# Kernel optimization log

Measured on AMD Instinct MI355X. Metric: run time of the kernel, lower is better.

## Reference

```python
import jax, jax.numpy as jnp
import numpy as np

M = 128      # max_child_num
H = 256      # hidden_size
F = 256      # node_feat_size (must equal H per original view logic)
T = 4        # edge_type_num
I = 2        # num_iterations
NSEM = 57    # Tree.num_sem


def setup_inputs() -> dict:
    key = jax.random.key(0)
    ks = jax.random.split(key, 16)
    def lin(k, shape, fan_in):
        return (jax.random.normal(k, shape, jnp.float32) / np.sqrt(fan_in)).astype(jnp.float32)
    return {
        "parent_feature": jax.random.normal(ks[0], (1, F), jnp.float32),
        "W_parent": lin(ks[1], (F, H * M), F),
        "b_parent": jnp.zeros((H * M,), jnp.float32),
        "W_exists": lin(ks[2], (H, 1), H),
        "b_exists": jnp.zeros((1,), jnp.float32),
        "W_edge_latent": lin(ks[3], (2 * H, H), 2 * H),
        "b_edge_latent": jnp.zeros((H,), jnp.float32),
        "W_edge_exists": lin(ks[4], (T, H), H),   # per-type 1-out linear, stacked
        "b_edge_exists": jnp.zeros((T,), jnp.float32),
        "W_op": lin(ks[5], (I, 3 * H + T, H), 3 * H + T),
        "b_op": jnp.zeros((I, H), jnp.float32),
        "W_child": lin(ks[6], (H * (I + 1), H), H * (I + 1)),
        "b_child": jnp.zeros((H,), jnp.float32),
        "W_sem": lin(ks[7], (H, NSEM), H),
        "b_sem": jnp.zeros((NSEM,), jnp.float32),
        "W_child2": lin(ks[8], (H, F), H),
        "b_child2": jnp.zeros((F,), jnp.float32),
    }


def reference(parent_feature, W_parent, b_parent, W_exists, b_exists,
              W_edge_latent, b_edge_latent, W_edge_exists, b_edge_exists,
              W_op, b_op, W_child, b_child, W_sem, b_sem, W_child2, b_child2):
    # parent -> per-child latents [M, H]
    cf = jax.nn.relu(parent_feature @ W_parent + b_parent).reshape(M, H)
    child_exists_logits = cf @ W_exists + b_exists                      # [M, 1]

    # pairwise edge latents [M, M, H]
    pair = jnp.concatenate([
        jnp.broadcast_to(cf[:, None, :], (M, M, H)),
        jnp.broadcast_to(cf[None, :, :], (M, M, H)),
    ], axis=-1)
    el = jax.nn.relu(pair @ W_edge_latent + b_edge_latent)              # [M, M, H]
    ee = jnp.einsum('ijh,th->ijt', el, W_edge_exists) + b_edge_exists   # [M, M, T]

    # dense-mask equivalent of torch.nonzero edge list: an edge exists per
    # (i, j, type) triple where its logit > 0 and both endpoints exist.
    exists = child_exists_logits[:, 0] > 0                              # [M]
    mask = (ee > 0) & exists[:, None, None] & exists[None, :, None]     # [M, M, T]
    maskf = mask.astype(cf.dtype)

    iter_feats = [cf]
    for i in range(I):
        # node_edge_op input is concat([cf_src, cf_dst, edge_latent, onehot(t)*logit]);
        # split the linear into per-block matmuls to avoid a [M,M,T,3H+T] concat.
        W1, W2, W3, W4 = (W_op[i, :H], W_op[i, H:2 * H],
                          W_op[i, 2 * H:3 * H], W_op[i, 3 * H:])        # W4: [T, H]
        pre = ((cf @ W1)[:, None, None, :]
               + (cf @ W2)[None, :, None, :]
               + (el @ W3)[:, :, None, :]
               + ee[:, :, :, None] * W4[None, None, :, :]
               + b_op[i])                                               # [M, M, T, H]
        h = jax.nn.relu(pre) * maskf[..., None]
        # scatter_max over source index i with zero-initialized output:
        # relu output >= 0 and masked-out edges are 0, so plain max matches.
        cf = jnp.max(h, axis=(1, 2))                                    # [M, H]
        iter_feats.append(cf)

    allf = jnp.concatenate(iter_feats, axis=1)                          # [M, H*(I+1)]
    ch = jax.nn.relu(allf @ W_child + b_child)                          # [M, H]
    child_sem_logits = ch @ W_sem + b_sem                               # [M, NSEM]
    child_feats = jax.nn.relu(ch @ W_child2 + b_child2)                 # [M, F]

    return (child_feats[None], child_sem_logits[None],
            child_exists_logits[None], ee[None])
```

## Files before the change

kernel.cpp:

```cpp
#include <hip/hip_runtime.h>
#include <hip/hip_bf16.h>

#define M_ 128
#define H_ 256
#define F_ 256
#define T_ 4
#define NSEM_ 57

typedef __attribute__((ext_vector_type(8))) short bf16x8;
typedef __attribute__((ext_vector_type(4))) float f32x4;

__device__ __forceinline__ float4 ld4(const float* p) { return *reinterpret_cast<const float4*>(p); }
__device__ __forceinline__ void st4(float* p, float4 v) { *reinterpret_cast<float4*>(p) = v; }
__device__ __forceinline__ float4 add4(float4 a, float4 b) { return make_float4(a.x+b.x, a.y+b.y, a.z+b.z, a.w+b.w); }
__device__ __forceinline__ float4 relu4(float4 a) { return make_float4(fmaxf(a.x,0.f), fmaxf(a.y,0.f), fmaxf(a.z,0.f), fmaxf(a.w,0.f)); }
__device__ __forceinline__ float4 fma4(float s, float4 w, float4 c) { return make_float4(fmaf(s,w.x,c.x), fmaf(s,w.y,c.y), fmaf(s,w.z,c.z), fmaf(s,w.w,c.w)); }

__device__ __forceinline__ unsigned short f2bfu(float x) {
  unsigned u = __float_as_uint(x);
  return (unsigned short)((u + 0x7FFFu + ((u >> 16) & 1u)) >> 16);
}
__device__ __forceinline__ unsigned pack2(float lo, float hi) {
  return (unsigned)f2bfu(lo) | ((unsigned)f2bfu(hi) << 16);
}

__global__ void __launch_bounds__(256) k_parent_partial(
    const float* __restrict__ pf, const float* __restrict__ Wp,
    float* __restrict__ part)
{
  const int cb = (blockIdx.x & 31) * 1024 + threadIdx.x * 4;
  const int kc = blockIdx.x >> 5;
  __shared__ float spf[16];
  if (threadIdx.x < 16) spf[threadIdx.x] = pf[kc * 16 + threadIdx.x];
  __syncthreads();
  const float* w = Wp + (size_t)kc * 16 * 32768 + cb;
  float4 acc = make_float4(0.f, 0.f, 0.f, 0.f);
  #pragma unroll
  for (int k = 0; k < 16; ++k)
    acc = fma4(spf[k], ld4(w + (size_t)k * 32768), acc);
  st4(&part[kc * 32768 + cb], acc);
}

__global__ void __launch_bounds__(256) k_stage1(
    const float* __restrict__ part, const float* __restrict__ bp,
    const float* __restrict__ Wel, const float* __restrict__ Wop0,
    const float* __restrict__ Wex, const float* __restrict__ bex,
    float* __restrict__ cf0, float* __restrict__ A, float* __restrict__ B,
    float* __restrict__ a1, float* __restrict__ a2,
    float* __restrict__ out_ex)
{
  const int m = blockIdx.x >> 1, sel = blockIdx.x & 1;
  const int t = threadIdx.x;
  __shared__ float sall[256];
  __shared__ float red[2][4][256];
  __shared__ float redE[4];

  float v = bp[m * 256 + t];
  #pragma unroll
  for (int q = 0; q < 16; ++q) v += part[q * 32768 + m * 256 + t];
  v = fmaxf(v, 0.f);
  sall[t] = v;
  if (sel == 0) {
    cf0[m * 256 + t] = v;
    float p = v * Wex[t];
    #pragma unroll
    for (int off = 32; off > 0; off >>= 1) p += __shfl_xor(p, off);
    if ((t & 63) == 0) redE[t >> 6] = p;
  }
  __syncthreads();

  const float* W0 = Wel  + (sel ? 65536 : 0);
  const float* W1 = Wop0 + (sel ? 65536 : 0);
  const int hq = (t & 63) << 2, kg = t >> 6, k0 = kg * 64;
  float4 acc0 = make_float4(0.f, 0.f, 0.f, 0.f), acc1 = acc0;
  #pragma unroll 4
  for (int k = k0; k < k0 + 64; ++k) {
    const float s = sall[k];
    acc0 = fma4(s, ld4(W0 + k * 256 + hq), acc0);
    acc1 = fma4(s, ld4(W1 + k * 256 + hq), acc1);
  }
  st4(&red[0][kg][hq], acc0);
  st4(&red[1][kg][hq], acc1);
  __syncthreads();
  if (kg < 2) {
    float4 r = add4(add4(ld4(&red[kg][0][hq]), ld4(&red[kg][1][hq])),
                    add4(ld4(&red[kg][2][hq]), ld4(&red[kg][3][hq])));
    float* dst = (kg == 0) ? (sel ? B : A) : (sel ? a2 : a1);
    st4(&dst[m * 256 + hq], r);
  }
  if (sel == 0 && t == 0)
    out_ex[m] = redE[0] + redE[1] + redE[2] + redE[3] + bex[0];
}

__global__ void __launch_bounds__(256) k_cvt_w(
    const float* __restrict__ Wop, unsigned short* __restrict__ W36F)
{
  const int fb = blockIdx.x;
  const int ct = fb >> 3, kc = fb & 7;
  #pragma unroll
  for (int r = 0; r < 2; ++r) {
    const int e = threadIdx.x * 2 + r;
    const int l = e >> 3, q = e & 7;
    const int c = ct * 16 + (l & 15);
    const int k = kc * 32 + (l >> 4) * 8 + q;
    const int it = c >> 8, h = c & 255;
    W36F[fb * 512 + e] = f2bfu(Wop[(size_t)it * 197632 + (512 + k) * 256 + h]);
  }
}

template<int IT>
__global__ void __launch_bounds__(512) k_gemm_epi(
    const float* __restrict__ Arow, const float* __restrict__ Brow,
    const float* __restrict__ bel, const unsigned short* __restrict__ W36F,
    const float* __restrict__ Wee, const float* __restrict__ bee,
    const float* __restrict__ a1, const float* __restrict__ a2,
    const float* __restrict__ Wop_it, const float* __restrict__ bop_it,
    const float* __restrict__ exlog,
    float* __restrict__ ee_g,
    float* __restrict__ part_op)
{
  const int i  = blockIdx.x >> 2;
  const int jq = blockIdx.x & 3;
  const int t  = threadIdx.x;
  const int w  = t >> 6;
  const int l  = t & 63;
  __shared__ char sEL[32 * 512];
  __shared__ float see[32][4];
  __shared__ float sexf[32];

  const bool exi = exlog[i] > 0.f;

  {
    const int row = t >> 4;
    const int sub = t & 15;
    const int kb  = sub * 16;
    const float* Ap  = Arow + i * 256 + kb;
    const float* Bp  = Brow + (jq * 32 + row) * 256 + kb;
    const float* blp = bel + kb;
    float e[16];
    #pragma unroll
    for (int q = 0; q < 16; q += 4) {
      float4 av = ld4(Ap + q), bv = ld4(Bp + q), lv = ld4(blp + q);
      e[q+0] = fmaxf(av.x + bv.x + lv.x, 0.f);
      e[q+1] = fmaxf(av.y + bv.y + lv.y, 0.f);
      e[q+2] = fmaxf(av.z + bv.z + lv.z, 0.f);
      e[q+3] = fmaxf(av.w + bv.w + lv.w, 0.f);
    }
    if (IT == 0) {
      float s[4] = {0.f, 0.f, 0.f, 0.f};
      #pragma unroll
      for (int tt = 0; tt < 4; ++tt) {
        #pragma unroll
        for (int q = 0; q < 16; q += 4) {
          float4 wv = ld4(Wee + tt * 256 + kb + q);
          s[tt] = fmaf(e[q+0], wv.x, s[tt]);
          s[tt] = fmaf(e[q+1], wv.y, s[tt]);
          s[tt] = fmaf(e[q+2], wv.z, s[tt]);
          s[tt] = fmaf(e[q+3], wv.w, s[tt]);
        }
      }
      #pragma unroll
      for (int off = 1; off < 16; off <<= 1) {
        s[0] += __shfl_xor(s[0], off);
        s[1] += __shfl_xor(s[1], off);
        s[2] += __shfl_xor(s[2], off);
        s[3] += __shfl_xor(s[3], off);
      }
      if (sub < 4) {
        const float v = s[sub] + bee[sub];
        see[row][sub] = v;
        ee_g[(i * 128 + jq * 32 + row) * 4 + sub] = v;
      }
    }
    const int swz = (row & 7) << 4;
    uint4 w0, w1;
    w0.x = pack2(e[0], e[1]);  w0.y = pack2(e[2], e[3]);
    w0.z = pack2(e[4], e[5]);  w0.w = pack2(e[6], e[7]);
    w1.x = pack2(e[8], e[9]);  w1.y = pack2(e[10], e[11]);
    w1.z = pack2(e[12], e[13]); w1.w = pack2(e[14], e[15]);
    *reinterpret_cast<uint4*>(sEL + ((row * 512 + kb * 2)      ^ swz)) = w0;
    *reinterpret_cast<uint4*>(sEL + ((row * 512 + kb * 2 + 16) ^ swz)) = w1;
  }
  if (IT == 1) {
    if (t < 128) see[t >> 2][t & 3] = ee_g[(i * 128 + jq * 32 + (t >> 2)) * 4 + (t & 3)];
  }
  if (t < 32) sexf[t] = exlog[jq * 32 + t];
  __syncthreads();

  const int lr = l & 15, lk = l >> 4;
  f32x4 acc[2][2];
  #pragma unroll
  for (int jt = 0; jt < 2; ++jt)
    #pragma unroll
    for (int ct = 0; ct < 2; ++ct)
      acc[jt][ct] = (f32x4){0.f, 0.f, 0.f, 0.f};

  for (int kc = 0; kc < 8; ++kc) {
    const int r0 = lr, r1 = 16 + lr;
    const int kbyte = kc * 64 + lk * 16;
    bf16x8 af0 = *reinterpret_cast<const bf16x8*>(
        sEL + ((r0 * 512 + kbyte) ^ ((r0 & 7) << 4)));
    bf16x8 af1 = *reinterpret_cast<const bf16x8*>(
        sEL + ((r1 * 512 + kbyte) ^ ((r1 & 7) << 4)));
    #pragma unroll
    for (int ct = 0; ct < 2; ++ct) {
      const int fb = (IT * 16 + w * 2 + ct) * 8 + kc;
      bf16x8 bf = *reinterpret_cast<const bf16x8*>(W36F + fb * 512 + l * 8);
      acc[0][ct] = __builtin_amdgcn_mfma_f32_16x16x32_bf16(af0, bf, acc[0][ct], 0, 0, 0);
      acc[1][ct] = __builtin_amdgcn_mfma_f32_16x16x32_bf16(af1, bf, acc[1][ct], 0, 0, 0);
    }
  }

  const int c0 = w * 32 + lr, c1 = c0 + 16;
  const float b10 = a1[i * 256 + c0] + bop_it[c0];
  const float b11 = a1[i * 256 + c1] + bop_it[c1];
  float w40[4], w41[4];
  #pragma unroll
  for (int tt = 0; tt < 4; ++tt) {
    w40[tt] = Wop_it[(768 + tt) * 256 + c0];
    w41[tt] = Wop_it[(768 + tt) * 256 + c1];
  }
  float am0 = 0.f, am1 = 0.f;
  #pragma unroll
  for (int jt = 0; jt < 2; ++jt) {
    #pragma unroll
    for (int q = 0; q < 4; ++q) {
      const int jrow = jt * 16 + lk * 4 + q;
      const int j = jq * 32 + jrow;
      if (exi && (sexf[jrow] > 0.f)) {
        const float e0 = see[jrow][0], e1 = see[jrow][1];
        const float e2 = see[jrow][2], e3 = see[jrow][3];
        const float pb0 = b10 + a2[j * 256 + c0] + acc[jt][0][q];
        const float pb1 = b11 + a2[j * 256 + c1] + acc[jt][1][q];
        if (e0 > 0.f) { am0 = fmaxf(am0, fmaxf(fmaf(e0, w40[0], pb0), 0.f));
                        am1 = fmaxf(am1, fmaxf(fmaf(e0, w41[0], pb1), 0.f)); }
        if (e1 > 0.f) { am0 = fmaxf(am0, fmaxf(fmaf(e1, w40[1], pb0), 0.f));
                        am1 = fmaxf(am1, fmaxf(fmaf(e1, w41[1], pb1), 0.f)); }
        if (e2 > 0.f) { am0 = fmaxf(am0, fmaxf(fmaf(e2, w40[2], pb0), 0.f));
                        am1 = fmaxf(am1, fmaxf(fmaf(e2, w41[2], pb1), 0.f)); }
        if (e3 > 0.f) { am0 = fmaxf(am0, fmaxf(fmaf(e3, w40[3], pb0), 0.f));
                        am1 = fmaxf(am1, fmaxf(fmaf(e3, w41[3], pb1), 0.f)); }
      }
    }
  }
  am0 = fmaxf(am0, __shfl_xor(am0, 16));
  am0 = fmaxf(am0, __shfl_xor(am0, 32));
  am1 = fmaxf(am1, __shfl_xor(am1, 16));
  am1 = fmaxf(am1, __shfl_xor(am1, 32));
  if (lk == 0) {
    part_op[(i * 4 + jq) * 256 + c0] = am0;
    part_op[(i * 4 + jq) * 256 + c1] = am1;
  }
}

__global__ void __launch_bounds__(256) k_a12b(
    const float* __restrict__ part_op, const float* __restrict__ Wop1,
    float* __restrict__ cf1, float* __restrict__ a1, float* __restrict__ a2)
{
  const int m = blockIdx.x >> 1, sel = blockIdx.x & 1;
  const int t = threadIdx.x;
  __shared__ float sall[256];
  __shared__ float red[4][256];
  float v = part_op[(m * 4 + 0) * 256 + t];
  v = fmaxf(v, part_op[(m * 4 + 1) * 256 + t]);
  v = fmaxf(v, part_op[(m * 4 + 2) * 256 + t]);
  v = fmaxf(v, part_op[(m * 4 + 3) * 256 + t]);
  sall[t] = v;
  if (sel == 0) cf1[m * 256 + t] = v;
  __syncthreads();
  const float* W = Wop1 + (sel ? 65536 : 0);
  const int hq = (t & 63) << 2, kg = t >> 6, k0 = kg * 64;
  float4 acc = make_float4(0.f, 0.f, 0.f, 0.f);
  #pragma unroll 4
  for (int k = k0; k < k0 + 64; ++k)
    acc = fma4(sall[k], ld4(W + k * 256 + hq), acc);
  st4(&red[kg][hq], acc);
  __syncthreads();
  if (kg == 0) {
    float4 r = add4(add4(ld4(&red[0][hq]), ld4(&red[1][hq])),
                    add4(ld4(&red[2][hq]), ld4(&red[3][hq])));
    st4(&((sel ? a2 : a1)[m * 256 + hq]), r);
  }
}

__global__ void __launch_bounds__(256) k_final(
    const float* __restrict__ cf0, const float* __restrict__ cf1,
    const float* __restrict__ part_op,
    const float* __restrict__ Wch, const float* __restrict__ bch,
    const float* __restrict__ Wsem, const float* __restrict__ bsem,
    const float* __restrict__ Wch2, const float* __restrict__ bch2,
    float* __restrict__ out_feats, float* __restrict__ out_sem)
{
  const int m  = blockIdx.x;
  const int t  = threadIdx.x;
  const int hq = (t & 63) << 2;
  const int kg = t >> 6;
  __shared__ float sall[768];
  __shared__ float sch[256];
  __shared__ float red[4][256];
  __shared__ float redS[4][64];

  sall[t]       = cf0[m * 256 + t];
  sall[256 + t] = cf1[m * 256 + t];
  {
    float v = part_op[(m * 4 + 0) * 256 + t];
    v = fmaxf(v, part_op[(m * 4 + 1) * 256 + t]);
    v = fmaxf(v, part_op[(m * 4 + 2) * 256 + t]);
    v = fmaxf(v, part_op[(m * 4 + 3) * 256 + t]);
    sall[512 + t] = v;
  }
  __syncthreads();

  {
    float4 acc = make_float4(0.f, 0.f, 0.f, 0.f);
    const int k0 = kg * 192;
    #pragma unroll 8
    for (int k = k0; k < k0 + 192; ++k)
      acc = fma4(sall[k], ld4(Wch + k * 256 + hq), acc);
    st4(&red[kg][hq], acc);
  }
  __syncthreads();
  if (kg == 0) {
    float4 r = add4(add4(ld4(&red[0][hq]), ld4(&red[1][hq])),
                    add4(ld4(&red[2][hq]), ld4(&red[3][hq])));
    r = relu4(add4(r, ld4(bch + hq)));
    st4(&sch[hq], r);
  }
  __syncthreads();

  {
    float4 f = make_float4(0.f, 0.f, 0.f, 0.f);
    const int k0 = kg * 64;
    #pragma unroll 8
    for (int k = k0; k < k0 + 64; ++k)
      f = fma4(sch[k], ld4(Wch2 + k * 256 + hq), f);
    const int s = t & 63;
    float sv = 0.f;
    if (s < 57) {
      #pragma unroll 8
      for (int k = k0; k < k0 + 64; ++k)
        sv = fmaf(sch[k], Wsem[k * 57 + s], sv);
    }
    redS[kg][s] = sv;
    __syncthreads();
    st4(&red[kg][hq], f);
  }
  __syncthreads();
  if (kg == 0) {
    float4 r = add4(add4(ld4(&red[0][hq]), ld4(&red[1][hq])),
                    add4(ld4(&red[2][hq]), ld4(&red[3][hq])));
    r = relu4(add4(r, ld4(bch2 + hq)));
    st4(&out_feats[m * 256 + hq], r);
    const int s = t & 63;
    if (s < 57)
      out_sem[m * 57 + s] = redS[0][s] + redS[1][s] + redS[2][s] + redS[3][s]
                          + bsem[s];
  }
}

extern "C" void kernel_launch(void* const* d_in, const int* in_sizes, int n_in,
                              void* d_out, int out_size, void* d_ws, size_t ws_size,
                              hipStream_t stream)
{
  const float* pf   = (const float*)d_in[0];
  const float* Wp   = (const float*)d_in[1];
  const float* bp   = (const float*)d_in[2];
  const float* Wex  = (const float*)d_in[3];
  const float* bex  = (const float*)d_in[4];
  const float* Wel  = (const float*)d_in[5];
  const float* bel  = (const float*)d_in[6];
  const float* Wee  = (const float*)d_in[7];
  const float* bee  = (const float*)d_in[8];
  const float* Wop  = (const float*)d_in[9];
  const float* bop  = (const float*)d_in[10];
  const float* Wch  = (const float*)d_in[11];
  const float* bch  = (const float*)d_in[12];
  const float* Wsem = (const float*)d_in[13];
  const float* bsem = (const float*)d_in[14];
  const float* Wch2 = (const float*)d_in[15];
  const float* bch2 = (const float*)d_in[16];

  float* out_feats = (float*)d_out;
  float* out_sem   = out_feats + M_ * F_;
  float* out_ex    = out_sem + M_ * NSEM_;
  float* out_ee    = out_ex + M_;

  float* ws = (float*)d_ws;
  float* cf0 = ws;
  float* cf1 = ws + 32768;
  float* Ab  = ws + 65536;
  float* Bb  = ws + 98304;
  float* a1  = ws + 131072;
  float* a2  = ws + 163840;
  float* part    = ws + 196608;
  float* part_op = ws + 196608;
  unsigned short* W36F = (unsigned short*)(ws + 720896);

  const float* Wop0 = Wop;
  const float* Wop1 = Wop + 197632;

  k_parent_partial<<<512, 256, 0, stream>>>(pf, Wp, part);
  k_stage1<<<256, 256, 0, stream>>>(part, bp, Wel, Wop0, Wex, bex,
                                    cf0, Ab, Bb, a1, a2, out_ex);
  k_cvt_w<<<256, 256, 0, stream>>>(Wop, W36F);

  k_gemm_epi<0><<<512, 512, 0, stream>>>(Ab, Bb, bel, W36F, Wee, bee,
                                         a1, a2, Wop0, bop, out_ex,
                                         out_ee, part_op);
  k_a12b<<<256, 256, 0, stream>>>(part_op, Wop1, cf1, a1, a2);
  k_gemm_epi<1><<<512, 512, 0, stream>>>(Ab, Bb, bel, W36F, Wee, bee,
                                         a1, a2, Wop1, bop + 256, out_ex,
                                         out_ee, part_op);
  k_final<<<128, 256, 0, stream>>>(cf0, cf1, part_op, Wch, bch, Wsem, bsem,
                                   Wch2, bch2, out_feats, out_sem);
}
```

Before: 71.12 us.

## Fuse weight conversion into parent kernel and fold iteration-1 projections into MFMA GEMM

Converts the W_op weights to bf16 inside the parent-projection kernel, whose grid is doubled by halving each block's K chunk. This removes the separate conversion launch. The k_a12b projection kernel is removed: iteration 1 now concatenates el, cf1[j] and cf1[i] into a K=768 bf16 MFMA GEMM, and per-row scatter-max results are combined with atomicMax on zero-initialised buffers instead of a partial array. This cuts two launches and a reduction pass, but triples the MFMA work of the second GEMM and adds atomics and extra bf16 rounding of cf1.

```diff
diff --git a/kernel.cpp b/kernel.cpp
--- a/kernel.cpp
+++ b/kernel.cpp
@@ -24,21 +24,41 @@
   return (unsigned)f2bfu(lo) | ((unsigned)f2bfu(hi) << 16);
 }
 
-__global__ void __launch_bounds__(256) k_parent_partial(
+__global__ void __launch_bounds__(256) k_parent(
     const float* __restrict__ pf, const float* __restrict__ Wp,
-    float* __restrict__ part)
+    const float* __restrict__ Wop, float* __restrict__ part,
+    unsigned short* __restrict__ W36F, unsigned short* __restrict__ W768F)
 {
   const int cb = (blockIdx.x & 31) * 1024 + threadIdx.x * 4;
   const int kc = blockIdx.x >> 5;
-  __shared__ float spf[16];
-  if (threadIdx.x < 16) spf[threadIdx.x] = pf[kc * 16 + threadIdx.x];
-  __syncthreads();
-  const float* w = Wp + (size_t)kc * 16 * 32768 + cb;
+  __shared__ float spf[8];
+  if (threadIdx.x < 8) spf[threadIdx.x] = pf[kc * 8 + threadIdx.x];
+  __syncthreads();
+  const float* w = Wp + (size_t)kc * 8 * 32768 + cb;
   float4 acc = make_float4(0.f, 0.f, 0.f, 0.f);
   #pragma unroll
-  for (int k = 0; k < 16; ++k)
+  for (int k = 0; k < 8; ++k)
     acc = fma4(spf[k], ld4(w + (size_t)k * 32768), acc);
   st4(&part[kc * 32768 + cb], acc);
+
+  const int g = blockIdx.x * 256 + threadIdx.x;
+  if (g < 65536) {
+    const int fb = g >> 9, e = g & 511;
+    const int kk = fb >> 4, ct = fb & 15;
+    const int l = e >> 3, q = e & 7;
+    const int k = kk * 32 + ((l >> 4) << 3) + q;
+    const int h = ct * 16 + (l & 15);
+    W36F[g] = f2bfu(Wop[(size_t)(512 + k) * 256 + h]);
+  } else {
+    const int g2 = g - 65536;
+    const int fb = g2 >> 9, e = g2 & 511;
+    const int kk = fb >> 4, ct = fb & 15;
+    const int l = e >> 3, q = e & 7;
+    const int k = kk * 32 + ((l >> 4) << 3) + q;
+    const int h = ct * 16 + (l & 15);
+    const int row = (k < 256) ? 512 + k : (k < 512 ? k : k - 512);
+    W768F[g2] = f2bfu(Wop[197632 + (size_t)row * 256 + h]);
+  }
 }
 
 __global__ void __launch_bounds__(256) k_stage1(
@@ -47,6 +67,7 @@
     const float* __restrict__ Wex, const float* __restrict__ bex,
     float* __restrict__ cf0, float* __restrict__ A, float* __restrict__ B,
     float* __restrict__ a1, float* __restrict__ a2,
+    float* __restrict__ cf1, float* __restrict__ cf2,
     float* __restrict__ out_ex)
 {
   const int m = blockIdx.x >> 1, sel = blockIdx.x & 1;
@@ -55,9 +76,11 @@
   __shared__ float red[2][4][256];
   __shared__ float redE[4];
 
+  (sel ? cf2 : cf1)[m * 256 + t] = 0.f;
+
   float v = bp[m * 256 + t];
-  #pragma unroll
-  for (int q = 0; q < 16; ++q) v += part[q * 32768 + m * 256 + t];
+  #pragma unroll 8
+  for (int q = 0; q < 32; ++q) v += part[q * 32768 + m * 256 + t];
   v = fmaxf(v, 0.f);
   sall[t] = v;
   if (sel == 0) {
@@ -92,32 +115,14 @@
     out_ex[m] = redE[0] + redE[1] + redE[2] + redE[3] + bex[0];
 }
 
-__global__ void __launch_bounds__(256) k_cvt_w(
-    const float* __restrict__ Wop, unsigned short* __restrict__ W36F)
-{
-  const int fb = blockIdx.x;
-  const int ct = fb >> 3, kc = fb & 7;
-  #pragma unroll
-  for (int r = 0; r < 2; ++r) {
-    const int e = threadIdx.x * 2 + r;
-    const int l = e >> 3, q = e & 7;
-    const int c = ct * 16 + (l & 15);
-    const int k = kc * 32 + (l >> 4) * 8 + q;
-    const int it = c >> 8, h = c & 255;
-    W36F[fb * 512 + e] = f2bfu(Wop[(size_t)it * 197632 + (512 + k) * 256 + h]);
-  }
-}
-
-template<int IT>
-__global__ void __launch_bounds__(512) k_gemm_epi(
+__global__ void __launch_bounds__(512) k_gemm0(
     const float* __restrict__ Arow, const float* __restrict__ Brow,
     const float* __restrict__ bel, const unsigned short* __restrict__ W36F,
     const float* __restrict__ Wee, const float* __restrict__ bee,
     const float* __restrict__ a1, const float* __restrict__ a2,
-    const float* __restrict__ Wop_it, const float* __restrict__ bop_it,
+    const float* __restrict__ Wop0, const float* __restrict__ bop0,
     const float* __restrict__ exlog,
-    float* __restrict__ ee_g,
-    float* __restrict__ part_op)
+    float* __restrict__ ee_g, float* __restrict__ cf1)
 {
   const int i  = blockIdx.x >> 2;
   const int jq = blockIdx.x & 3;
@@ -146,31 +151,29 @@
       e[q+2] = fmaxf(av.z + bv.z + lv.z, 0.f);
       e[q+3] = fmaxf(av.w + bv.w + lv.w, 0.f);
     }
-    if (IT == 0) {
-      float s[4] = {0.f, 0.f, 0.f, 0.f};
+    float s[4] = {0.f, 0.f, 0.f, 0.f};
+    #pragma unroll
+    for (int tt = 0; tt < 4; ++tt) {
       #pragma unroll
-      for (int tt = 0; tt < 4; ++tt) {
-        #pragma unroll
-        for (int q = 0; q < 16; q += 4) {
-          float4 wv = ld4(Wee + tt * 256 + kb + q);
-          s[tt] = fmaf(e[q+0], wv.x, s[tt]);
-          s[tt] = fmaf(e[q+1], wv.y, s[tt]);
-          s[tt] = fmaf(e[q+2], wv.z, s[tt]);
-          s[tt] = fmaf(e[q+3], wv.w, s[tt]);
-        }
+      for (int q = 0; q < 16; q += 4) {
+        float4 wv = ld4(Wee + tt * 256 + kb + q);
+        s[tt] = fmaf(e[q+0], wv.x, s[tt]);
+        s[tt] = fmaf(e[q+1], wv.y, s[tt]);
+        s[tt] = fmaf(e[q+2], wv.z, s[tt]);
+        s[tt] = fmaf(e[q+3], wv.w, s[tt]);
       }
-      #pragma unroll
-      for (int off = 1; off < 16; off <<= 1) {
-        s[0] += __shfl_xor(s[0], off);
-        s[1] += __shfl_xor(s[1], off);
-        s[2] += __shfl_xor(s[2], off);
-        s[3] += __shfl_xor(s[3], off);
-      }
-      if (sub < 4) {
-        const float v = s[sub] + bee[sub];
-        see[row][sub] = v;
-        ee_g[(i * 128 + jq * 32 + row) * 4 + sub] = v;
-      }
+    }
+    #pragma unroll
+    for (int off = 1; off < 16; off <<= 1) {
+      s[0] += __shfl_xor(s[0], off);
+      s[1] += __shfl_xor(s[1], off);
+      s[2] += __shfl_xor(s[2], off);
+      s[3] += __shfl_xor(s[3], off);
+    }
+    if (sub < 4) {
+      const float v = s[sub] + bee[sub];
+      see[row][sub] = v;
+      ee_g[(i * 128 + jq * 32 + row) * 4 + sub] = v;
     }
     const int swz = (row & 7) << 4;
     uint4 w0, w1;
@@ -181,9 +184,6 @@
     *reinterpret_cast<uint4*>(sEL + ((row * 512 + kb * 2)      ^ swz)) = w0;
     *reinterpret_cast<uint4*>(sEL + ((row * 512 + kb * 2 + 16) ^ swz)) = w1;
   }
-  if (IT == 1) {
-    if (t < 128) see[t >> 2][t & 3] = ee_g[(i * 128 + jq * 32 + (t >> 2)) * 4 + (t & 3)];
-  }
   if (t < 32) sexf[t] = exlog[jq * 32 + t];
   __syncthreads();
 
@@ -196,15 +196,14 @@
       acc[jt][ct] = (f32x4){0.f, 0.f, 0.f, 0.f};
 
   for (int kc = 0; kc < 8; ++kc) {
-    const int r0 = lr, r1 = 16 + lr;
     const int kbyte = kc * 64 + lk * 16;
     bf16x8 af0 = *reinterpret_cast<const bf16x8*>(
-        sEL + ((r0 * 512 + kbyte) ^ ((r0 & 7) << 4)));
+        sEL + ((lr * 512 + kbyte) ^ ((lr & 7) << 4)));
     bf16x8 af1 = *reinterpret_cast<const bf16x8*>(
-        sEL + ((r1 * 512 + kbyte) ^ ((r1 & 7) << 4)));
+        sEL + (((16 + lr) * 512 + kbyte) ^ ((lr & 7) << 4)));
     #pragma unroll
     for (int ct = 0; ct < 2; ++ct) {
-      const int fb = (IT * 16 + w * 2 + ct) * 8 + kc;
+      const int fb = kc * 16 + (w * 2 + ct);
       bf16x8 bf = *reinterpret_cast<const bf16x8*>(W36F + fb * 512 + l * 8);
       acc[0][ct] = __builtin_amdgcn_mfma_f32_16x16x32_bf16(af0, bf, acc[0][ct], 0, 0, 0);
       acc[1][ct] = __builtin_amdgcn_mfma_f32_16x16x32_bf16(af1, bf, acc[1][ct], 0, 0, 0);
@@ -212,13 +211,13 @@
   }
 
   const int c0 = w * 32 + lr, c1 = c0 + 16;
-  const float b10 = a1[i * 256 + c0] + bop_it[c0];
-  const float b11 = a1[i * 256 + c1] + bop_it[c1];
+  const float b10 = a1[i * 256 + c0] + bop0[c0];
+  const float b11 = a1[i * 256 + c1] + bop0[c1];
   float w40[4], w41[4];
   #pragma unroll
   for (int tt = 0; tt < 4; ++tt) {
-    w40[tt] = Wop_it[(768 + tt) * 256 + c0];
-    w41[tt] = Wop_it[(768 + tt) * 256 + c1];
+    w40[tt] = Wop0[(768 + tt) * 256 + c0];
+    w41[tt] = Wop0[(768 + tt) * 256 + c1];
   }
   float am0 = 0.f, am1 = 0.f;
   #pragma unroll
@@ -248,44 +247,151 @@
   am1 = fmaxf(am1, __shfl_xor(am1, 16));
   am1 = fmaxf(am1, __shfl_xor(am1, 32));
   if (lk == 0) {
-    part_op[(i * 4 + jq) * 256 + c0] = am0;
-    part_op[(i * 4 + jq) * 256 + c1] = am1;
-  }
-}
-
-__global__ void __launch_bounds__(256) k_a12b(
-    const float* __restrict__ part_op, const float* __restrict__ Wop1,
-    float* __restrict__ cf1, float* __restrict__ a1, float* __restrict__ a2)
+    atomicMax((unsigned int*)&cf1[i * 256 + c0], __float_as_uint(am0));
+    atomicMax((unsigned int*)&cf1[i * 256 + c1], __float_as_uint(am1));
+  }
+}
+
+__global__ void __launch_bounds__(512) k_gemm1(
+    const float* __restrict__ Arow, const float* __restrict__ Brow,
+    const float* __restrict__ bel, const unsigned short* __restrict__ W768F,
+    const float* __restrict__ cf1,
+    const float* __restrict__ Wop1, const float* __restrict__ bop1,
+    const float* __restrict__ exlog, const float* __restrict__ ee_g,
+    float* __restrict__ cf2)
 {
-  const int m = blockIdx.x >> 1, sel = blockIdx.x & 1;
-  const int t = threadIdx.x;
-  __shared__ float sall[256];
-  __shared__ float red[4][256];
-  float v = part_op[(m * 4 + 0) * 256 + t];
-  v = fmaxf(v, part_op[(m * 4 + 1) * 256 + t]);
-  v = fmaxf(v, part_op[(m * 4 + 2) * 256 + t]);
-  v = fmaxf(v, part_op[(m * 4 + 3) * 256 + t]);
-  sall[t] = v;
-  if (sel == 0) cf1[m * 256 + t] = v;
-  __syncthreads();
-  const float* W = Wop1 + (sel ? 65536 : 0);
-  const int hq = (t & 63) << 2, kg = t >> 6, k0 = kg * 64;
-  float4 acc = make_float4(0.f, 0.f, 0.f, 0.f);
-  #pragma unroll 4
-  for (int k = k0; k < k0 + 64; ++k)
-    acc = fma4(sall[k], ld4(W + k * 256 + hq), acc);
-  st4(&red[kg][hq], acc);
-  __syncthreads();
-  if (kg == 0) {
-    float4 r = add4(add4(ld4(&red[0][hq]), ld4(&red[1][hq])),
-                    add4(ld4(&red[2][hq]), ld4(&red[3][hq])));
-    st4(&((sel ? a2 : a1)[m * 256 + hq]), r);
+  const int i  = blockIdx.x >> 2;
+  const int jq = blockIdx.x & 3;
+  const int t  = threadIdx.x;
+  const int w  = t >> 6;
+  const int l  = t & 63;
+  __shared__ char sEL[32 * 1536];
+  __shared__ float see[32][4];
+  __shared__ float sexf[32];
+
+  const bool exi = exlog[i] > 0.f;
+
+  {
+    const int row = t >> 4;
+    const int sub = t & 15;
+    const int kb  = sub * 16;
+    const int swz = (row & 7) << 4;
+    {
+      const float* Ap  = Arow + i * 256 + kb;
+      const float* Bp  = Brow + (jq * 32 + row) * 256 + kb;
+      const float* blp = bel + kb;
+      float e[16];
+      #pragma unroll
+      for (int q = 0; q < 16; q += 4) {
+        float4 av = ld4(Ap + q), bv = ld4(Bp + q), lv = ld4(blp + q);
+        e[q+0] = fmaxf(av.x + bv.x + lv.x, 0.f);
+        e[q+1] = fmaxf(av.y + bv.y + lv.y, 0.f);
+        e[q+2] = fmaxf(av.z + bv.z + lv.z, 0.f);
+        e[q+3] = fmaxf(av.w + bv.w + lv.w, 0.f);
+      }
+      uint4 w0, w1;
+      w0.x = pack2(e[0], e[1]);  w0.y = pack2(e[2], e[3]);
+      w0.z = pack2(e[4], e[5]);  w0.w = pack2(e[6], e[7]);
+      w1.x = pack2(e[8], e[9]);  w1.y = pack2(e[10], e[11]);
+      w1.z = pack2(e[12], e[13]); w1.w = pack2(e[14], e[15]);
+      *reinterpret_cast<uint4*>(sEL + ((row * 1536 + kb * 2)      ^ swz)) = w0;
+      *reinterpret_cast<uint4*>(sEL + ((row * 1536 + kb * 2 + 16) ^ swz)) = w1;
+    }
+    {
+      const float* cj = cf1 + (jq * 32 + row) * 256 + kb;
+      float4 v0 = ld4(cj), v1 = ld4(cj + 4), v2 = ld4(cj + 8), v3 = ld4(cj + 12);
+      uint4 w0, w1;
+      w0.x = pack2(v0.x, v0.y); w0.y = pack2(v0.z, v0.w);
+      w0.z = pack2(v1.x, v1.y); w0.w = pack2(v1.z, v1.w);
+      w1.x = pack2(v2.x, v2.y); w1.y = pack2(v2.z, v2.w);
+      w1.z = pack2(v3.x, v3.y); w1.w = pack2(v3.z, v3.w);
+      *reinterpret_cast<uint4*>(sEL + ((row * 1536 + 512 + kb * 2)      ^ swz)) = w0;
+      *reinterpret_cast<uint4*>(sEL + ((row * 1536 + 512 + kb * 2 + 16) ^ swz)) = w1;
+    }
+    {
+      const float* ci = cf1 + i * 256 + kb;
+      float4 v0 = ld4(ci), v1 = ld4(ci + 4), v2 = ld4(ci + 8), v3 = ld4(ci + 12);
+      uint4 w0, w1;
+      w0.x = pack2(v0.x, v0.y); w0.y = pack2(v0.z, v0.w);
+      w0.z = pack2(v1.x, v1.y); w0.w = pack2(v1.z, v1.w);
+      w1.x = pack2(v2.x, v2.y); w1.y = pack2(v2.z, v2.w);
+      w1.z = pack2(v3.x, v3.y); w1.w = pack2(v3.z, v3.w);
+      *reinterpret_cast<uint4*>(sEL + ((row * 1536 + 1024 + kb * 2)      ^ swz)) = w0;
+      *reinterpret_cast<uint4*>(sEL + ((row * 1536 + 1024 + kb * 2 + 16) ^ swz)) = w1;
+    }
+  }
+  if (t < 128)
+    see[t >> 2][t & 3] = ee_g[(i * 128 + jq * 32 + (t >> 2)) * 4 + (t & 3)];
+  if (t < 32) sexf[t] = exlog[jq * 32 + t];
+  __syncthreads();
+
+  const int lr = l & 15, lk = l >> 4;
+  f32x4 acc[2][2];
+  #pragma unroll
+  for (int jt = 0; jt < 2; ++jt)
+    #pragma unroll
+    for (int ct = 0; ct < 2; ++ct)
+      acc[jt][ct] = (f32x4){0.f, 0.f, 0.f, 0.f};
+
+  for (int kc = 0; kc < 24; ++kc) {
+    const int kbyte = kc * 64 + lk * 16;
+    bf16x8 af0 = *reinterpret_cast<const bf16x8*>(
+        sEL + ((lr * 1536 + kbyte) ^ ((lr & 7) << 4)));
+    bf16x8 af1 = *reinterpret_cast<const bf16x8*>(
+        sEL + (((16 + lr) * 1536 + kbyte) ^ ((lr & 7) << 4)));
+    #pragma unroll
+    for (int ct = 0; ct < 2; ++ct) {
+      const int fb = kc * 16 + (w * 2 + ct);
+      bf16x8 bf = *reinterpret_cast<const bf16x8*>(W768F + fb * 512 + l * 8);
+      acc[0][ct] = __builtin_amdgcn_mfma_f32_16x16x32_bf16(af0, bf, acc[0][ct], 0, 0, 0);
+      acc[1][ct] = __builtin_amdgcn_mfma_f32_16x16x32_bf16(af1, bf, acc[1][ct], 0, 0, 0);
+    }
+  }
+
+  const int c0 = w * 32 + lr, c1 = c0 + 16;
+  const float b10 = bop1[c0];
+  const float b11 = bop1[c1];
+  float w40[4], w41[4];
+  #pragma unroll
+  for (int tt = 0; tt < 4; ++tt) {
+    w40[tt] = Wop1[(768 + tt) * 256 + c0];
+    w41[tt] = Wop1[(768 + tt) * 256 + c1];
+  }
+  float am0 = 0.f, am1 = 0.f;
+  #pragma unroll
+  for (int jt = 0; jt < 2; ++jt) {
+    #pragma unroll
+    for (int q = 0; q < 4; ++q) {
+      const int jrow = jt * 16 + lk * 4 + q;
+      if (exi && (sexf[jrow] > 0.f)) {
+        const float e0 = see[jrow][0], e1 = see[jrow][1];
+        const float e2 = see[jrow][2], e3 = see[jrow][3];
+        const float pb0 = b10 + acc[jt][0][q];
+        const float pb1 = b11 + acc[jt][1][q];
+        if (e0 > 0.f) { am0 = fmaxf(am0, fmaxf(fmaf(e0, w40[0], pb0), 0.f));
+                        am1 = fmaxf(am1, fmaxf(fmaf(e0, w41[0], pb1), 0.f)); }
+        if (e1 > 0.f) { am0 = fmaxf(am0, fmaxf(fmaf(e1, w40[1], pb0), 0.f));
+                        am1 = fmaxf(am1, fmaxf(fmaf(e1, w41[1], pb1), 0.f)); }
+        if (e2 > 0.f) { am0 = fmaxf(am0, fmaxf(fmaf(e2, w40[2], pb0), 0.f));
+                        am1 = fmaxf(am1, fmaxf(fmaf(e2, w41[2], pb1), 0.f)); }
+        if (e3 > 0.f) { am0 = fmaxf(am0, fmaxf(fmaf(e3, w40[3], pb0), 0.f));
+                        am1 = fmaxf(am1, fmaxf(fmaf(e3, w41[3], pb1), 0.f)); }
+      }
+    }
+  }
+  am0 = fmaxf(am0, __shfl_xor(am0, 16));
+  am0 = fmaxf(am0, __shfl_xor(am0, 32));
+  am1 = fmaxf(am1, __shfl_xor(am1, 16));
+  am1 = fmaxf(am1, __shfl_xor(am1, 32));
+  if (lk == 0) {
+    atomicMax((unsigned int*)&cf2[i * 256 + c0], __float_as_uint(am0));
+    atomicMax((unsigned int*)&cf2[i * 256 + c1], __float_as_uint(am1));
   }
 }
 
 __global__ void __launch_bounds__(256) k_final(
     const float* __restrict__ cf0, const float* __restrict__ cf1,
-    const float* __restrict__ part_op,
+    const float* __restrict__ cf2,
     const float* __restrict__ Wch, const float* __restrict__ bch,
     const float* __restrict__ Wsem, const float* __restrict__ bsem,
     const float* __restrict__ Wch2, const float* __restrict__ bch2,
@@ -302,13 +408,7 @@
 
   sall[t]       = cf0[m * 256 + t];
   sall[256 + t] = cf1[m * 256 + t];
-  {
-    float v = part_op[(m * 4 + 0) * 256 + t];
-    v = fmaxf(v, part_op[(m * 4 + 1) * 256 + t]);
-    v = fmaxf(v, part_op[(m * 4 + 2) * 256 + t]);
-    v = fmaxf(v, part_op[(m * 4 + 3) * 256 + t]);
-    sall[512 + t] = v;
-  }
+  sall[512 + t] = cf2[m * 256 + t];
   __syncthreads();
 
   {
@@ -388,29 +488,25 @@
   float* ws = (float*)d_ws;
   float* cf0 = ws;
   float* cf1 = ws + 32768;
-  float* Ab  = ws + 65536;
-  float* Bb  = ws + 98304;
-  float* a1  = ws + 131072;
-  float* a2  = ws + 163840;
-  float* part    = ws + 196608;
-  float* part_op = ws + 196608;
-  unsigned short* W36F = (unsigned short*)(ws + 720896);
+  float* cf2 = ws + 65536;
+  float* Ab  = ws + 98304;
+  float* Bb  = ws + 131072;
+  float* a1  = ws + 163840;
+  float* a2  = ws + 196608;
+  float* part = ws + 229376;
+  unsigned short* W36F  = (unsigned short*)(ws + 1277952);
+  unsigned short* W768F = (unsigned short*)(ws + 1310720);
 
   const float* Wop0 = Wop;
   const float* Wop1 = Wop + 197632;
 
-  k_parent_partial<<<512, 256, 0, stream>>>(pf, Wp, part);
+  k_parent<<<1024, 256, 0, stream>>>(pf, Wp, Wop, part, W36F, W768F);
   k_stage1<<<256, 256, 0, stream>>>(part, bp, Wel, Wop0, Wex, bex,
-                                    cf0, Ab, Bb, a1, a2, out_ex);
-  k_cvt_w<<<256, 256, 0, stream>>>(Wop, W36F);
-
-  k_gemm_epi<0><<<512, 512, 0, stream>>>(Ab, Bb, bel, W36F, Wee, bee,
-                                         a1, a2, Wop0, bop, out_ex,
-                                         out_ee, part_op);
-  k_a12b<<<256, 256, 0, stream>>>(part_op, Wop1, cf1, a1, a2);
-  k_gemm_epi<1><<<512, 512, 0, stream>>>(Ab, Bb, bel, W36F, Wee, bee,
-                                         a1, a2, Wop1, bop + 256, out_ex,
-                                         out_ee, part_op);
-  k_final<<<128, 256, 0, stream>>>(cf0, cf1, part_op, Wch, bch, Wsem, bsem,
+                                    cf0, Ab, Bb, a1, a2, cf1, cf2, out_ex);
+  k_gemm0<<<512, 512, 0, stream>>>(Ab, Bb, bel, W36F, Wee, bee,
+                                   a1, a2, Wop0, bop, out_ex, out_ee, cf1);
+  k_gemm1<<<512, 512, 0, stream>>>(Ab, Bb, bel, W768F, cf1,
+                                   Wop1, bop + 256, out_ex, out_ee, cf2);
+  k_final<<<128, 256, 0, stream>>>(cf0, cf1, cf2, Wch, bch, Wsem, bsem,
                                    Wch2, bch2, out_feats, out_sem);
 }
```

After: 68.88 us. 1.03x faster.
